# Kernel tuning notes

Measured on AMD Instinct MI355X. Metric: run time of the kernel, lower is better.

## Reference

```python
import jax, jax.numpy as jnp
import numpy as np
import math


def _rotate_one(kernel, angle):
    """Bilinear-rotate one group kernel [Cg,Cg,kH,kW] by scalar angle."""
    kH, kW = kernel.shape[2], kernel.shape[3]
    cy, cx = (kH - 1) / 2.0, (kW - 1) / 2.0
    y = jnp.arange(kH, dtype=kernel.dtype) - cy
    x = jnp.arange(kW, dtype=kernel.dtype) - cx
    yy, xx = jnp.meshgrid(y, x, indexing='ij')
    c, s = jnp.cos(angle), jnp.sin(angle)
    x_rot = xx * c + yy * s + cx
    y_rot = -xx * s + yy * c + cy
    x0 = jnp.clip(jnp.floor(x_rot), 0, kW - 2)
    y0 = jnp.clip(jnp.floor(y_rot), 0, kH - 2)
    x1 = x0 + 1
    y1 = y0 + 1
    w00 = (x1 - x_rot) * (y1 - y_rot)
    w01 = (x1 - x_rot) * (y_rot - y0)
    w10 = (x_rot - x0) * (y1 - y_rot)
    w11 = (x_rot - x0) * (y_rot - y0)
    x0i = x0.astype(jnp.int32); y0i = y0.astype(jnp.int32)
    x1i = x1.astype(jnp.int32); y1i = y1.astype(jnp.int32)
    # gather over last two dims: [Cg,Cg,kH,kW]
    return (w00 * kernel[..., y0i, x0i] + w01 * kernel[..., y1i, x0i]
            + w10 * kernel[..., y0i, x1i] + w11 * kernel[..., y1i, x1i])


def setup_inputs() -> dict:
    key = jax.random.key(0)
    ks = jax.random.split(key, 6)
    B, C, H, W = 16, 256, 64, 64
    G, Cg, K = 8, 32, 3
    HID = C // 4  # 64
    fan_out = Cg * K * K
    return {
        'x': jax.random.normal(ks[0], (B, C, H, W), jnp.float32),
        'base_kernel': jax.random.normal(ks[1], (G, Cg, Cg, K, K), jnp.float32) * np.sqrt(2.0 / fan_out),
        'ap_w1': jax.random.normal(ks[2], (HID, C), jnp.float32) * np.sqrt(1.0 / C),
        'ap_b1': jnp.zeros((HID,), jnp.float32),
        'ap_w2': jax.random.normal(ks[3], (G, HID), jnp.float32) * np.sqrt(1.0 / HID),
        'ap_b2': jnp.zeros((G,), jnp.float32),
        'meta_w1': jax.random.normal(ks[4], (HID, C), jnp.float32) * np.sqrt(1.0 / C),
        'meta_b1': jnp.zeros((HID,), jnp.float32),
        'meta_w2': jax.random.normal(ks[5], (C, HID), jnp.float32) * np.sqrt(1.0 / HID),
        'meta_b2': jnp.zeros((C,), jnp.float32),
    }


def reference(x, base_kernel, ap_w1, ap_b1, ap_w2, ap_b2,
              meta_w1, meta_b1, meta_w2, meta_b2):
    B, C, H, W = x.shape
    G, Cg = base_kernel.shape[0], base_kernel.shape[1]
    K = base_kernel.shape[-1]
    pad = (K - 1) // 2

    pooled = x.mean(axis=(2, 3))  # [B,C] == AdaptiveAvgPool2d(1) on 1x1-conv MLPs

    # angle predictor: 1x1 conv MLP -> tanh -> scale by pi/4
    h = jax.nn.relu(pooled @ ap_w1.T + ap_b1)
    angles = jnp.tanh(h @ ap_w2.T + ap_b2) * (math.pi / 4)  # [B,G]

    # per-(sample,group) bilinear kernel rotation, fully vectorized
    rot = jax.vmap(jax.vmap(_rotate_one), in_axes=(None, 0))(base_kernel, angles)
    # rot: [B,G,Cg,Cg,K,K] -> per-sample grouped conv via feature_group_count=B*G
    w = rot.reshape(B * C, Cg, K, K)
    out = jax.lax.conv_general_dilated(
        x.reshape(1, B * C, H, W), w, window_strides=(1, 1),
        padding=[(pad, pad), (pad, pad)],
        dimension_numbers=('NCHW', 'OIHW', 'NCHW'),
        feature_group_count=B * G)
    feat = out.reshape(B, C, H, W)

    # meta modulation: squeeze-excite style gate
    m = jax.nn.relu(pooled @ meta_w1.T + meta_b1)
    mod = jax.nn.sigmoid(m @ meta_w2.T + meta_b2)  # [B,C]
    return feat * mod[:, :, None, None]
```

## Files before the change

### kernel.cpp

```cpp
#include <hip/hip_runtime.h>
#include <math.h>

#define B_ 16
#define C_ 256
#define H_ 64
#define W_ 64
#define G_ 8
#define CG_ 32
#define HID_ 64

typedef __attribute__((ext_vector_type(8))) short short8;
typedef __attribute__((ext_vector_type(4))) float floatx4;

__device__ inline unsigned short f2bf(float f) {
    union { float f; unsigned u; } v; v.f = f;
    unsigned r = v.u + 0x7fffu + ((v.u >> 16) & 1u);
    return (unsigned short)(r >> 16);
}

__device__ __forceinline__ void gld16(const unsigned short* g, unsigned short* l) {
    __builtin_amdgcn_global_load_lds(
        (const __attribute__((address_space(1))) unsigned int*)g,
        (__attribute__((address_space(3))) unsigned int*)l, 16, 0, 0);
}

__global__ void xpose_pool(const float* __restrict__ x,
                           unsigned short* __restrict__ xT,
                           float* __restrict__ rowsum) {
    int bid = blockIdx.x;
    int tid = threadIdx.x;
    int w = tid & 63, q = tid >> 6;
    int h = bid & 63, bg = bid >> 6;

    const float* src = x + (((size_t)bg * 32 + q * 8) * 64 + h) * 64 + w;
    float v[8];
#pragma unroll
    for (int j = 0; j < 8; ++j) v[j] = src[(size_t)j * 4096];

    short8 sv;
#pragma unroll
    for (int j = 0; j < 8; ++j) sv[j] = (short)f2bf(v[j]);
    *(short8*)(xT + ((size_t)(bid * 4 + q) * 64 + w) * 8) = sv;

#pragma unroll
    for (int j = 0; j < 8; ++j) {
#pragma unroll
        for (int off = 32; off > 0; off >>= 1) v[j] += __shfl_down(v[j], off, 64);
    }
    if (w == 0) {
        float* rs = rowsum + (size_t)bid * 32 + q * 8;
#pragma unroll
        for (int j = 0; j < 8; ++j) rs[j] = v[j];
    }
}

__global__ void mlp_kernel(const float* __restrict__ rowsum,
                           const float* __restrict__ ap_w1, const float* __restrict__ ap_b1,
                           const float* __restrict__ ap_w2, const float* __restrict__ ap_b2,
                           const float* __restrict__ mw1, const float* __restrict__ mb1,
                           const float* __restrict__ mw2, const float* __restrict__ mb2,
                           float* __restrict__ angles, float* __restrict__ modg) {
    int b = blockIdx.x, tid = threadIdx.x;
    __shared__ __align__(16) float sp[C_];
    __shared__ __align__(16) float ha[HID_], hm[HID_];

    {
        const float* rs = rowsum + ((size_t)(b * 8 + (tid >> 5)) * 64) * 32 + (tid & 31);
        float s = 0.f;
#pragma unroll
        for (int h = 0; h < 64; ++h) s += rs[h * 32];
        sp[tid] = s * (1.0f / 4096.0f);
    }
    __syncthreads();

    if (tid < 64) {
        const float4* wr = (const float4*)(ap_w1 + tid * C_);
        const float4* p4 = (const float4*)sp;
        float s = ap_b1[tid];
#pragma unroll
        for (int i = 0; i < 64; ++i) {
            float4 wv = wr[i], pv = p4[i];
            s = fmaf(pv.x, wv.x, s); s = fmaf(pv.y, wv.y, s);
            s = fmaf(pv.z, wv.z, s); s = fmaf(pv.w, wv.w, s);
        }
        ha[tid] = fmaxf(s, 0.f);
    } else if (tid < 128) {
        int t = tid - 64;
        const float4* wr = (const float4*)(mw1 + t * C_);
        const float4* p4 = (const float4*)sp;
        float s = mb1[t];
#pragma unroll
        for (int i = 0; i < 64; ++i) {
            float4 wv = wr[i], pv = p4[i];
            s = fmaf(pv.x, wv.x, s); s = fmaf(pv.y, wv.y, s);
            s = fmaf(pv.z, wv.z, s); s = fmaf(pv.w, wv.w, s);
        }
        hm[t] = fmaxf(s, 0.f);
    }
    __syncthreads();

    if (tid < G_) {
        const float* wr = ap_w2 + tid * HID_;
        float s = ap_b2[tid];
        for (int i = 0; i < HID_; ++i) s = fmaf(ha[i], wr[i], s);
        angles[b * G_ + tid] = tanhf(s) * 0.78539816339744830962f;
    }
    {
        const float* wr = mw2 + tid * HID_;
        float s = mb2[tid];
        for (int i = 0; i < HID_; ++i) s = fmaf(hm[i], wr[i], s);
        modg[b * C_ + tid] = 1.0f / (1.0f + expf(-s));
    }
}

__global__ void rot_kernel(const float* __restrict__ base, const float* __restrict__ angles,
                           unsigned short* __restrict__ rotw) {
    int e = blockIdx.x * 256 + threadIdx.x;
    int ci = e & 31;
    int co = (e >> 5) & 31;
    int t = e >> 10;
    int k = t % 9;
    int bg = t / 9;
    int b = bg >> 3, g = bg & 7;

    float ang = angles[b * G_ + g];
    float cc = __cosf(ang), ss = __sinf(ang);
    int i = k / 3, j = k % 3;
    float fx = (float)(j - 1), fy = (float)(i - 1);
    float xr = fx * cc + fy * ss + 1.0f;
    float yr = -fx * ss + fy * cc + 1.0f;
    float x0f = fminf(fmaxf(floorf(xr), 0.f), 1.f);
    float y0f = fminf(fmaxf(floorf(yr), 0.f), 1.f);
    float w00 = (x0f + 1.f - xr) * (y0f + 1.f - yr);
    float w01 = (x0f + 1.f - xr) * (yr - y0f);
    float w10 = (xr - x0f) * (y0f + 1.f - yr);
    float w11 = (xr - x0f) * (yr - y0f);
    int x0 = (int)x0f, y0 = (int)y0f;

    const float* bk = base + (((size_t)(g * CG_ + co) * CG_ + ci) * 9);
    float v = w00 * bk[y0 * 3 + x0] + w01 * bk[(y0 + 1) * 3 + x0] +
              w10 * bk[y0 * 3 + x0 + 1] + w11 * bk[(y0 + 1) * 3 + x0 + 1];
    rotw[e] = f2bf(v);
}

__global__ __launch_bounds__(256, 2) void conv_mfma(const unsigned short* __restrict__ xT,
                                                    const unsigned short* __restrict__ rotw,
                                                    const float* __restrict__ modg,
                                                    float* __restrict__ out) {
    __shared__ __align__(16) unsigned short sW[9 * 32 * 32];
    __shared__ __align__(16) unsigned short sX[10 * 4 * 66 * 8];
    __shared__ float smod[32];
    int bg = blockIdx.x;
    int b = bg >> 3, g = bg & 7;
    int r0 = blockIdx.y * 8;
    int tid = threadIdx.x;
    int lane = tid & 63;
    int wv = tid >> 6;

#pragma unroll
    for (int i = 0; i < 5; ++i) {
        int idx = tid + i * 256;
        if (idx < 1152)
            gld16(rotw + (size_t)bg * 9216 + idx * 8, &sW[idx * 8]);
    }

#pragma unroll
    for (int i = 0; i < 10; ++i) {
        int s = wv + i * 4;
        int r = s >> 2, q = s & 3;
        int grow = r0 - 1 + r;
        unsigned short* lp = &sX[((size_t)s * 66 + 1 + lane) * 8];
        if (grow >= 0 && grow < H_) {
            gld16(xT + ((((size_t)bg * 64 + grow) * 4 + q) * 64 + lane) * 8, lp);
        } else {
            *(short8*)lp = (short8){0, 0, 0, 0, 0, 0, 0, 0};
        }
    }
    if (tid < 80) {
        int s = tid >> 1, side = tid & 1;
        *(short8*)&sX[((size_t)s * 66 + side * 65) * 8] = (short8){0, 0, 0, 0, 0, 0, 0, 0};
    }
    if (tid < 32) smod[tid] = modg[b * C_ + g * CG_ + tid];
    __syncthreads();

    int nlo = lane & 15;
    int quad = lane >> 4;

    floatx4 acc0[8], acc1[8];
#pragma unroll
    for (int nt = 0; nt < 8; ++nt) {
        acc0[nt] = (floatx4){0.f, 0.f, 0.f, 0.f};
        acc1[nt] = (floatx4){0.f, 0.f, 0.f, 0.f};
    }

#pragma unroll
    for (int k9 = 0; k9 < 9; ++k9) {
        const int dy = k9 / 3 - 1, dx = k9 % 3 - 1;
        short8 a0 = *(const short8*)&sW[((k9 * 32) + nlo) * 32 + quad * 8];
        short8 a1 = *(const short8*)&sW[((k9 * 32) + 16 + nlo) * 32 + quad * 8];
#pragma unroll
        for (int nt = 0; nt < 8; ++nt) {
            int rr = wv * 2 + (nt >> 2) + 1 + dy;
            int cc = (nt & 3) * 16 + nlo + 1 + dx;
            short8 bf = *(const short8*)&sX[(((size_t)rr * 4 + quad) * 66 + cc) * 8];
            acc0[nt] = __builtin_amdgcn_mfma_f32_16x16x32_bf16(a0, bf, acc0[nt], 0, 0, 0);
            acc1[nt] = __builtin_amdgcn_mfma_f32_16x16x32_bf16(a1, bf, acc1[nt], 0, 0, 0);
        }
    }

    float gm[2][4];
#pragma unroll
    for (int mt = 0; mt < 2; ++mt)
#pragma unroll
        for (int reg = 0; reg < 4; ++reg) gm[mt][reg] = smod[mt * 16 + quad * 4 + reg];

#pragma unroll
    for (int nt = 0; nt < 8; ++nt) {
        int row = r0 + wv * 2 + (nt >> 2);
        int col = (nt & 3) * 16 + nlo;
#pragma unroll
        for (int reg = 0; reg < 4; ++reg) {
            int co0 = quad * 4 + reg;
            out[((size_t)(b * C_ + g * CG_ + co0) * H_ + row) * W_ + col] = acc0[nt][reg] * gm[0][reg];
            int co1 = 16 + quad * 4 + reg;
            out[((size_t)(b * C_ + g * CG_ + co1) * H_ + row) * W_ + col] = acc1[nt][reg] * gm[1][reg];
        }
    }
}

extern "C" void kernel_launch(void* const* d_in, const int* in_sizes, int n_in,
                              void* d_out, int out_size, void* d_ws, size_t ws_size,
                              hipStream_t stream) {
    const float* x      = (const float*)d_in[0];
    const float* basek  = (const float*)d_in[1];
    const float* ap_w1  = (const float*)d_in[2];
    const float* ap_b1  = (const float*)d_in[3];
    const float* ap_w2  = (const float*)d_in[4];
    const float* ap_b2  = (const float*)d_in[5];
    const float* mw1    = (const float*)d_in[6];
    const float* mb1    = (const float*)d_in[7];
    const float* mw2    = (const float*)d_in[8];
    const float* mb2    = (const float*)d_in[9];
    float* out = (float*)d_out;

    float* wsf    = (float*)d_ws;
    float* rowsum = wsf;
    float* angles = wsf + 262144;
    float* modg   = wsf + 262272;
    unsigned short* rotw = (unsigned short*)(wsf + 266368);
    unsigned short* xT   = (unsigned short*)(wsf + 856192);

    xpose_pool<<<B_ * G_ * H_, 256, 0, stream>>>(x, xT, rowsum);
    mlp_kernel<<<B_, 256, 0, stream>>>(rowsum, ap_w1, ap_b1, ap_w2, ap_b2,
                                       mw1, mb1, mw2, mb2, angles, modg);
    rot_kernel<<<(B_ * G_ * CG_ * CG_ * 9) / 256, 256, 0, stream>>>(basek, angles, rotw);
    dim3 cgrid(B_ * G_, H_ / 8);
    conv_mfma<<<cgrid, 256, 0, stream>>>(xT, rotw, modg, out);
}
```

Baseline: 163.5 us.

## Reuse input fragments across kernel rows in conv, stage pool reduction in LDS, nontemporal IO

The conv inner loop now loads each input-row fragment set once into registers and reuses it across the three kernel rows with double buffering, replacing 72 LDS reads per wave with 48. The MLP kernel stages the rowsum block into LDS with async global-to-LDS loads before reducing it. The transpose loads and the conv output stores become nontemporal to avoid polluting the cache, and the modulation load is issued earlier. The changes raise register pressure from 24 live short8 fragments, which may hurt occupancy under launch_bounds(256,2).

```diff
diff --git a/kernel.cpp b/kernel.cpp
--- a/kernel.cpp
+++ b/kernel.cpp
@@ -18,7 +18,7 @@
     return (unsigned short)(r >> 16);
 }
 
-__device__ __forceinline__ void gld16(const unsigned short* g, unsigned short* l) {
+__device__ __forceinline__ void gld16(const void* g, void* l) {
     __builtin_amdgcn_global_load_lds(
         (const __attribute__((address_space(1))) unsigned int*)g,
         (__attribute__((address_space(3))) unsigned int*)l, 16, 0, 0);
@@ -35,7 +35,7 @@
     const float* src = x + (((size_t)bg * 32 + q * 8) * 64 + h) * 64 + w;
     float v[8];
 #pragma unroll
-    for (int j = 0; j < 8; ++j) v[j] = src[(size_t)j * 4096];
+    for (int j = 0; j < 8; ++j) v[j] = __builtin_nontemporal_load(&src[(size_t)j * 4096]);
 
     short8 sv;
 #pragma unroll
@@ -61,55 +61,68 @@
                            const float* __restrict__ mw2, const float* __restrict__ mb2,
                            float* __restrict__ angles, float* __restrict__ modg) {
     int b = blockIdx.x, tid = threadIdx.x;
+    __shared__ __align__(16) float sL[8192];
     __shared__ __align__(16) float sp[C_];
     __shared__ __align__(16) float ha[HID_], hm[HID_];
 
-    {
-        const float* rs = rowsum + ((size_t)(b * 8 + (tid >> 5)) * 64) * 32 + (tid & 31);
-        float s = 0.f;
-#pragma unroll
-        for (int h = 0; h < 64; ++h) s += rs[h * 32];
-        sp[tid] = s * (1.0f / 4096.0f);
-    }
+    const float* rs = rowsum + (size_t)b * 16384;
+    float s = 0.f;
+#pragma unroll
+    for (int p = 0; p < 2; ++p) {
+#pragma unroll
+        for (int i = 0; i < 8; ++i) {
+            int chunk = tid + i * 256;
+            gld16(rs + (size_t)p * 8192 + chunk * 4, &sL[chunk * 4]);
+        }
+        __syncthreads();
+        if ((tid >> 7) == p) {
+            int gl = (tid >> 5) & 3, ci = tid & 31;
+            const float* base = &sL[gl * 2048 + ci];
+#pragma unroll
+            for (int h = 0; h < 64; ++h) s += base[h * 32];
+        }
+        __syncthreads();
+    }
+    sp[tid] = s * (1.0f / 4096.0f);
     __syncthreads();
 
     if (tid < 64) {
         const float4* wr = (const float4*)(ap_w1 + tid * C_);
         const float4* p4 = (const float4*)sp;
-        float s = ap_b1[tid];
+        float s2 = ap_b1[tid];
 #pragma unroll
         for (int i = 0; i < 64; ++i) {
             float4 wv = wr[i], pv = p4[i];
-            s = fmaf(pv.x, wv.x, s); s = fmaf(pv.y, wv.y, s);
-            s = fmaf(pv.z, wv.z, s); s = fmaf(pv.w, wv.w, s);
-        }
-        ha[tid] = fmaxf(s, 0.f);
+            s2 = fmaf(pv.x, wv.x, s2); s2 = fmaf(pv.y, wv.y, s2);
+            s2 = fmaf(pv.z, wv.z, s2); s2 = fmaf(pv.w, wv.w, s2);
+        }
+        ha[tid] = fmaxf(s2, 0.f);
     } else if (tid < 128) {
         int t = tid - 64;
         const float4* wr = (const float4*)(mw1 + t * C_);
         const float4* p4 = (const float4*)sp;
-        float s = mb1[t];
+        float s2 = mb1[t];
 #pragma unroll
         for (int i = 0; i < 64; ++i) {
             float4 wv = wr[i], pv = p4[i];
-            s = fmaf(pv.x, wv.x, s); s = fmaf(pv.y, wv.y, s);
-            s = fmaf(pv.z, wv.z, s); s = fmaf(pv.w, wv.w, s);
-        }
-        hm[t] = fmaxf(s, 0.f);
+            s2 = fmaf(pv.x, wv.x, s2); s2 = fmaf(pv.y, wv.y, s2);
+            s2 = fmaf(pv.z, wv.z, s2); s2 = fmaf(pv.w, wv.w, s2);
+        }
+        hm[t] = fmaxf(s2, 0.f);
     }
     __syncthreads();
 
     if (tid < G_) {
         const float* wr = ap_w2 + tid * HID_;
-        float s = ap_b2[tid];
-        for (int i = 0; i < HID_; ++i) s = fmaf(ha[i], wr[i], s);
-        angles[b * G_ + tid] = tanhf(s) * 0.78539816339744830962f;
+        float s2 = ap_b2[tid];
+        for (int i = 0; i < HID_; ++i) s2 = fmaf(ha[i], wr[i], s2);
+        angles[b * G_ + tid] = tanhf(s2) * 0.78539816339744830962f;
     }
     {
         const float* wr = mw2 + tid * HID_;
-        float s = mb2[tid];
-        for (int i = 0; i < HID_; ++i) s = fmaf(hm[i], wr[i], s);
-        modg[b * C_ + tid] = 1.0f / (1.0f + expf(-s));
+        float s2 = mb2[tid];
+        for (int i = 0; i < HID_; ++i) s2 = fmaf(hm[i], wr[i], s2);
+        modg[b * C_ + tid] = 1.0f / (1.0f + expf(-s2));
     }
 }
 
@@ -143,6 +156,33 @@
     rotw[e] = f2bf(v);
 }
 
+__device__ __forceinline__ void loadF(short8 (&F)[12], const unsigned short* pB, int trow) {
+#pragma unroll
+    for (int ct = 0; ct < 4; ++ct)
+#pragma unroll
+        for (int dxx = 0; dxx < 3; ++dxx)
+            F[ct * 3 + dxx] = *(const short8*)(pB + trow * 2112 + ct * 128 + dxx * 8 - 8);
+}
+
+__device__ __forceinline__ void phase(floatx4 (&acc0)[8], floatx4 (&acc1)[8],
+                                      const short8 (&F0)[12], const short8 (&F1)[12],
+                                      const unsigned short* sW, int k9b, int nlo, int quad) {
+#pragma unroll
+    for (int dxx = 0; dxx < 3; ++dxx) {
+        int k9 = k9b + dxx;
+        short8 a0 = *(const short8*)&sW[((k9 * 32) + nlo) * 32 + quad * 8];
+        short8 a1 = *(const short8*)&sW[((k9 * 32) + 16 + nlo) * 32 + quad * 8];
+#pragma unroll
+        for (int ct = 0; ct < 4; ++ct) {
+            int fi = ct * 3 + dxx;
+            acc0[ct]     = __builtin_amdgcn_mfma_f32_16x16x32_bf16(a0, F0[fi], acc0[ct], 0, 0, 0);
+            acc1[ct]     = __builtin_amdgcn_mfma_f32_16x16x32_bf16(a1, F0[fi], acc1[ct], 0, 0, 0);
+            acc0[4 + ct] = __builtin_amdgcn_mfma_f32_16x16x32_bf16(a0, F1[fi], acc0[4 + ct], 0, 0, 0);
+            acc1[4 + ct] = __builtin_amdgcn_mfma_f32_16x16x32_bf16(a1, F1[fi], acc1[4 + ct], 0, 0, 0);
+        }
+    }
+}
+
 __global__ __launch_bounds__(256, 2) void conv_mfma(const unsigned short* __restrict__ xT,
                                                     const unsigned short* __restrict__ rotw,
                                                     const float* __restrict__ modg,
@@ -157,6 +197,8 @@
     int lane = tid & 63;
     int wv = tid >> 6;
 
+    if (tid < 32) smod[tid] = modg[b * C_ + g * CG_ + tid];
+
 #pragma unroll
     for (int i = 0; i < 5; ++i) {
         int idx = tid + i * 256;
@@ -180,7 +222,6 @@
         int s = tid >> 1, side = tid & 1;
         *(short8*)&sX[((size_t)s * 66 + side * 65) * 8] = (short8){0, 0, 0, 0, 0, 0, 0, 0};
     }
-    if (tid < 32) smod[tid] = modg[b * C_ + g * CG_ + tid];
     __syncthreads();
 
     int nlo = lane & 15;
@@ -193,20 +234,16 @@
         acc1[nt] = (floatx4){0.f, 0.f, 0.f, 0.f};
     }
 
-#pragma unroll
-    for (int k9 = 0; k9 < 9; ++k9) {
-        const int dy = k9 / 3 - 1, dx = k9 % 3 - 1;
-        short8 a0 = *(const short8*)&sW[((k9 * 32) + nlo) * 32 + quad * 8];
-        short8 a1 = *(const short8*)&sW[((k9 * 32) + 16 + nlo) * 32 + quad * 8];
-#pragma unroll
-        for (int nt = 0; nt < 8; ++nt) {
-            int rr = wv * 2 + (nt >> 2) + 1 + dy;
-            int cc = (nt & 3) * 16 + nlo + 1 + dx;
-            short8 bf = *(const short8*)&sX[(((size_t)rr * 4 + quad) * 66 + cc) * 8];
-            acc0[nt] = __builtin_amdgcn_mfma_f32_16x16x32_bf16(a0, bf, acc0[nt], 0, 0, 0);
-            acc1[nt] = __builtin_amdgcn_mfma_f32_16x16x32_bf16(a1, bf, acc1[nt], 0, 0, 0);
-        }
-    }
+    const unsigned short* pB = &sX[((size_t)(wv * 8 + quad) * 66 + nlo + 1) * 8];
+
+    short8 Fa[12], Fb[12];
+    loadF(Fa, pB, 0);
+    loadF(Fb, pB, 1);
+    phase(acc0, acc1, Fa, Fb, sW, 0, nlo, quad);
+    loadF(Fa, pB, 2);
+    phase(acc0, acc1, Fb, Fa, sW, 3, nlo, quad);
+    loadF(Fb, pB, 3);
+    phase(acc0, acc1, Fa, Fb, sW, 6, nlo, quad);
 
     float gm[2][4];
 #pragma unroll
@@ -221,9 +258,11 @@
 #pragma unroll
         for (int reg = 0; reg < 4; ++reg) {
             int co0 = quad * 4 + reg;
-            out[((size_t)(b * C_ + g * CG_ + co0) * H_ + row) * W_ + col] = acc0[nt][reg] * gm[0][reg];
+            __builtin_nontemporal_store(acc0[nt][reg] * gm[0][reg],
+                &out[((size_t)(b * C_ + g * CG_ + co0) * H_ + row) * W_ + col]);
             int co1 = 16 + quad * 4 + reg;
-            out[((size_t)(b * C_ + g * CG_ + co1) * H_ + row) * W_ + col] = acc1[nt][reg] * gm[1][reg];
+            __builtin_nontemporal_store(acc1[nt][reg] * gm[1][reg],
+                &out[((size_t)(b * C_ + g * CG_ + co1) * H_ + row) * W_ + col]);
         }
     }
 }
```

After: 169.8 us. 3.8% more time.
